# Performance work log

Hardware: AMD Instinct MI355X
Metric: run time of the kernel (lower is better)

Reference implementation:

```python
import jax, jax.numpy as jnp
import numpy as np

N_SRC = 100000
N_DST = 50000
N_EDGES = 1000000
D = 64
N_CLASSES = 64


def setup_inputs() -> dict:
    key = jax.random.key(0)
    ks = jax.random.split(key, 6)
    x = jax.random.normal(ks[0], (N_SRC, D), dtype=jnp.float32)
    w = jax.random.uniform(ks[1], (N_EDGES,), dtype=jnp.float32)
    u_sum = jax.random.uniform(ks[2], (N_SRC,), dtype=jnp.float32)
    W_w = jax.random.normal(ks[3], (N_CLASSES, 2 * D), dtype=jnp.float32) * (1.0 / np.sqrt(2 * D))
    W_b = jax.random.normal(ks[4], (N_CLASSES,), dtype=jnp.float32) * 0.01
    src_idx = jax.random.randint(ks[5], (N_EDGES,), 0, N_SRC, dtype=jnp.int64 if jax.config.jax_enable_x64 else jnp.int32)
    dst_idx = jax.random.randint(jax.random.fold_in(key, 7), (N_EDGES,), 0, N_DST, dtype=jnp.int64 if jax.config.jax_enable_x64 else jnp.int32)
    return {"x": x, "w": w, "u_sum": u_sum, "W_w": W_w, "W_b": W_b,
            "src_idx": src_idx, "dst_idx": dst_idx, "n_dst": N_DST}


def reference(x, w, u_sum, W_w, W_b, src_idx, dst_idx, n_dst):
    n_src, d = x.shape
    out_dim = W_w.shape[0]
    x_dst = x[:n_dst]                                  # dstdata['x']
    msgs = x[src_idx]                                  # [E, d] gather (u)
    # First update_all: u_mul_e + sum. NOTE: in the original module this result
    # is immediately overwritten by the second update_all, so it is dead math;
    # computed here for structural fidelity (XLA will DCE it).
    y_wsum = jax.ops.segment_sum(msgs * w[:, None], dst_idx, num_segments=n_dst)
    # Second update_all: copy_u + mean -> this is the 'y' actually used.
    deg = jax.ops.segment_sum(jnp.ones_like(w), dst_idx, num_segments=n_dst)
    y_mean = jax.ops.segment_sum(msgs, dst_idx, num_segments=n_dst) / jnp.maximum(deg, 1.0)[:, None]
    h = jnp.concatenate([x_dst, y_mean], axis=1) @ W_w.T + W_b  # [n_dst, out_dim]
    mean_x = jnp.mean(y_mean, axis=0)                  # [d]
    mean_u = u_sum / n_dst                             # [n_src]
    diff = mean_u[:, None] * x - mean_x                # [n_src, d]
    reg_loss = jnp.sum(diff * diff) / (n_src * out_dim)
    return h, reg_loss
```

## Files before the change

kernel.cpp:

```cpp
#include <hip/hip_runtime.h>

#define N_SRC   100000
#define N_DSTC  50000
#define N_EDGES 1000000
#define DIM     64
#define NCLS    64

#define SCAN_BPB 256
#define SCAN_NB  ((N_DSTC + SCAN_BPB - 1) / SCAN_BPB)

#define HIST_BLOCKS ((N_EDGES / 4 + 255) / 256)
#define REG_BLOCKS  1024
#define GATHER_GRID 1024


__global__ __launch_bounds__(256) void hist_reg_kernel(
    const int4*  __restrict__ dst4,
    const float* __restrict__ x,
    const float* __restrict__ u_sum,
    int*   __restrict__ hist,
    float* __restrict__ regA,
    float* __restrict__ regB) {
  __shared__ float redB[4][64];
  __shared__ float redA[4];

  if (blockIdx.x < HIST_BLOCKS) {
    int i = blockIdx.x * blockDim.x + threadIdx.x;
    if (i < N_EDGES / 4) {
      int4 d = dst4[i];
      atomicAdd(&hist[d.x], 1);
      atomicAdd(&hist[d.y], 1);
      atomicAdd(&hist[d.z], 1);
      atomicAdd(&hist[d.w], 1);
    }
    return;
  }

  const int tid  = threadIdx.x;
  const int wv   = tid >> 6;
  const int lane = tid & 63;
  const int waveId     = (blockIdx.x - HIST_BLOCKS) * 4 + wv;
  const int totalWaves = REG_BLOCKS * 4;

  float accA = 0.0f;
  float accB = 0.0f;
  for (int r = waveId; r < N_SRC; r += totalWaves) {
    float u  = u_sum[r];
    float xv = x[r * DIM + lane];
    float t  = u * xv;
    accB += t;
    accA = fmaf(t, t, accA);
  }
  #pragma unroll
  for (int off = 32; off > 0; off >>= 1)
    accA += __shfl_down(accA, off, 64);
  if (lane == 0) redA[wv] = accA;
  redB[wv][lane] = accB;
  __syncthreads();
  if (tid < 64) {
    float b = redB[0][tid] + redB[1][tid] + redB[2][tid] + redB[3][tid];
    atomicAdd(&regB[tid], b);
  }
  if (tid == 0) {
    float a = redA[0] + redA[1] + redA[2] + redA[3];
    atomicAdd(regA, a);
  }
}

__global__ __launch_bounds__(256) void scan_local(
    const int* __restrict__ hist, int* __restrict__ cursor,
    int* __restrict__ blockSums) {
  __shared__ int A[256], B[256];
  const int b = blockIdx.x, t = threadIdx.x;
  const int g = b * SCAN_BPB + t;
  int v = (g < N_DSTC) ? hist[g] : 0;
  A[t] = v;
  __syncthreads();
  int* cur = A; int* nxt = B;
  for (int off = 1; off < 256; off <<= 1) {
    int s = cur[t] + ((t >= off) ? cur[t - off] : 0);
    nxt[t] = s;
    __syncthreads();
    int* tmp = cur; cur = nxt; nxt = tmp;
  }
  if (g < N_DSTC) cursor[g] = cur[t] - v;
  if (t == 255) blockSums[b] = cur[255];
}

__global__ __launch_bounds__(256) void scan_addoff(
    int* __restrict__ cursor, const int* __restrict__ blockSums) {
  __shared__ int A[256], B[256];
  const int b = blockIdx.x, t = threadIdx.x;
  A[t] = (t < SCAN_NB) ? blockSums[t] : 0;
  __syncthreads();
  int* cur = A; int* nxt = B;
  for (int off = 1; off < 256; off <<= 1) {
    int s = cur[t] + ((t >= off) ? cur[t - off] : 0);
    nxt[t] = s;
    __syncthreads();
    int* tmp = cur; cur = nxt; nxt = tmp;
  }
  int off = (b > 0) ? cur[b - 1] : 0;
  int g = b * SCAN_BPB + t;
  if (g < N_DSTC) cursor[g] += off;
}

__global__ __launch_bounds__(256) void reorder_kernel(
    const int4* __restrict__ src4, const int4* __restrict__ dst4,
    int* __restrict__ cursor, int* __restrict__ sorted_src) {
  int i = blockIdx.x * blockDim.x + threadIdx.x;
  if (i < N_EDGES / 4) {
    int4 s = src4[i];
    int4 d = dst4[i];
    int p0 = atomicAdd(&cursor[d.x], 1); sorted_src[p0] = s.x;
    int p1 = atomicAdd(&cursor[d.y], 1); sorted_src[p1] = s.y;
    int p2 = atomicAdd(&cursor[d.z], 1); sorted_src[p2] = s.z;
    int p3 = atomicAdd(&cursor[d.w], 1); sorted_src[p3] = s.w;
  }
}

__global__ __launch_bounds__(256, 4) void gather_h(
    const float* __restrict__ x,
    const float* __restrict__ Ww,
    const float* __restrict__ Wb,
    const int*   __restrict__ cursor,
    const int*   __restrict__ sorted_src,
    float* __restrict__ h,
    float* __restrict__ colsum,
    float* __restrict__ regA,
    float* __restrict__ regB,
    int*   __restrict__ doneG,
    float* __restrict__ out_scalar) {
  __shared__ float Wt[2 * DIM][NCLS + 1];
  __shared__ float colred[4][64];
  __shared__ int   lastFlag;

  const int tid = threadIdx.x;
  for (int idx = tid; idx < NCLS * 2 * DIM; idx += 256) {
    int c = idx >> 7, k = idx & 127;
    Wt[k][c] = Ww[idx];
  }
  __syncthreads();

  const int wv   = tid >> 6;
  const int lane = tid & 63;
  const int es   = lane >> 4;
  const int q    = lane & 15;
  const int waveId = blockIdx.x * 4 + wv;
  const int tw     = gridDim.x * 4;
  const float bias = Wb[lane];
  const float4* x4 = reinterpret_cast<const float4*>(x);

  float4 colacc = make_float4(0.f, 0.f, 0.f, 0.f);

  for (int r = waveId; r < N_DSTC; r += tw) {
    int beg = (r == 0) ? 0 : cursor[r - 1];
    int end = cursor[r];
    int cnt = end - beg;

    float4 a = make_float4(0.f, 0.f, 0.f, 0.f);
    for (int base = 0; base < cnt; base += 64) {
      int rem = cnt - base;
      int mm  = rem < 64 ? rem : 64;
      int idxv = (lane < rem) ? sorted_src[beg + base + lane] : 0;

      int jb = 0;
      for (; jb + 8 <= mm; jb += 8) {
        int s0 = __shfl(idxv, jb + es,     64);
        int s1 = __shfl(idxv, jb + 4 + es, 64);
        float4 v0 = x4[s0 * 16 + q];
        float4 v1 = x4[s1 * 16 + q];
        a.x += v0.x + v1.x;
        a.y += v0.y + v1.y;
        a.z += v0.z + v1.z;
        a.w += v0.w + v1.w;
      }
      for (; jb < mm; jb += 4) {
        int j = jb + es;
        int s0 = __shfl(idxv, j & 63, 64);
        if (j < mm) {
          float4 v = x4[s0 * 16 + q];
          a.x += v.x; a.y += v.y; a.z += v.z; a.w += v.w;
        }
      }
    }
    a.x += __shfl_xor(a.x, 16, 64); a.y += __shfl_xor(a.y, 16, 64);
    a.z += __shfl_xor(a.z, 16, 64); a.w += __shfl_xor(a.w, 16, 64);
    a.x += __shfl_xor(a.x, 32, 64); a.y += __shfl_xor(a.y, 32, 64);
    a.z += __shfl_xor(a.z, 32, 64); a.w += __shfl_xor(a.w, 32, 64);

    float inv = 1.0f / fmaxf((float)cnt, 1.0f);
    float4 ym = make_float4(a.x * inv, a.y * inv, a.z * inv, a.w * inv);

    float4 xv = x4[r * 16 + q];

    if (es == 0) {
      colacc.x += ym.x; colacc.y += ym.y; colacc.z += ym.z; colacc.w += ym.w;
    }

    float hacc = bias;
    #pragma unroll
    for (int k = 0; k < DIM; ++k) {
      const int sl = k >> 2;
      float fx = __shfl((k & 3) == 0 ? xv.x : (k & 3) == 1 ? xv.y :
                        (k & 3) == 2 ? xv.z : xv.w, sl, 64);
      float fy = __shfl((k & 3) == 0 ? ym.x : (k & 3) == 1 ? ym.y :
                        (k & 3) == 2 ? ym.z : ym.w, sl, 64);
      hacc = fmaf(fx, Wt[k][lane], hacc);
      hacc = fmaf(fy, Wt[DIM + k][lane], hacc);
    }
    h[r * NCLS + lane] = hacc;
  }

  if (es == 0) {
    colred[wv][q * 4 + 0] = colacc.x;
    colred[wv][q * 4 + 1] = colacc.y;
    colred[wv][q * 4 + 2] = colacc.z;
    colred[wv][q * 4 + 3] = colacc.w;
  }
  __syncthreads();
  if (tid < 64) {
    float s = colred[0][tid] + colred[1][tid] + colred[2][tid] + colred[3][tid];
    atomicAdd(&colsum[tid], s);
  }

  __syncthreads();
  if (tid == 0) {
    __threadfence();
    int old = atomicAdd(doneG, 1);
    lastFlag = (old == (int)gridDim.x - 1) ? 1 : 0;
  }
  __syncthreads();
  if (lastFlag && tid < 64) {
    const float inv_nd = 1.0f / (float)N_DSTC;
    float cs = atomicAdd(&colsum[tid], 0.0f);
    float bv = atomicAdd(&regB[tid], 0.0f);
    float mx = cs * inv_nd;
    float p = fmaf((float)N_SRC * mx, mx, -2.0f * inv_nd * mx * bv);
    #pragma unroll
    for (int off = 32; off > 0; off >>= 1)
      p += __shfl_down(p, off, 64);
    if (tid == 0) {
      float av = atomicAdd(regA, 0.0f);
      float total = fmaf(av, inv_nd * inv_nd, p);
      out_scalar[0] = total * (1.0f / ((float)N_SRC * (float)NCLS));
    }
  }
}

extern "C" void kernel_launch(void* const* d_in, const int* in_sizes, int n_in,
                              void* d_out, int out_size, void* d_ws, size_t ws_size,
                              hipStream_t stream) {
  const float* x     = (const float*)d_in[0];
  const float* u_sum = (const float*)d_in[2];
  const float* Ww    = (const float*)d_in[3];
  const float* Wb    = (const float*)d_in[4];
  const int*   src   = (const int*)d_in[5];
  const int*   dst   = (const int*)d_in[6];

  float* out = (float*)d_out;
  int*   wsI = (int*)d_ws;

  int*   hist       = wsI;
  float* colsum     = (float*)(wsI + N_DSTC);
  float* regA       = colsum + 64;
  float* regB       = regA + 1;
  int*   doneG      = (int*)(regB + 64);
  int*   blockSums  = doneG + 1;
  int*   cursor     = blockSums + SCAN_NB;
  int*   sorted_src = cursor + N_DSTC;

  hipMemsetAsync(d_ws, 0, (size_t)(N_DSTC + 64 + 1 + 64 + 1) * sizeof(int), stream);

  hist_reg_kernel<<<HIST_BLOCKS + REG_BLOCKS, 256, 0, stream>>>(
      (const int4*)dst, x, u_sum, hist, regA, regB);
  scan_local  <<<SCAN_NB, 256, 0, stream>>>(hist, cursor, blockSums);
  scan_addoff <<<SCAN_NB, 256, 0, stream>>>(cursor, blockSums);
  reorder_kernel<<<(N_EDGES / 4 + 255) / 256, 256, 0, stream>>>(
      (const int4*)src, (const int4*)dst, cursor, sorted_src);
  gather_h    <<<GATHER_GRID, 256, 0, stream>>>(
      x, Ww, Wb, cursor, sorted_src, out, colsum, regA, regB, doneG,
      out + (size_t)N_DSTC * NCLS);
}
```

Before: 392.6 us.

## Gather neighbor features from a bf16 copy of x built in the reg pass

The reg-loss pass now also writes a round-to-nearest bf16 copy of x into workspace. The gather kernel reads that copy with 8 lanes per row and 8 rows per wave-step, which halves the bytes fetched per edge. It then reduces across lanes and redistributes one feature per lane before the linear layer. The gather grid is also doubled. The copy adds a write of about 12.8 MB, and summing bf16 values adds rounding error to the mean.

```diff
diff --git a/kernel.cpp b/kernel.cpp
--- a/kernel.cpp
+++ b/kernel.cpp
@@ -11,7 +11,7 @@
 
 #define HIST_BLOCKS ((N_EDGES / 4 + 255) / 256)
 #define REG_BLOCKS  1024
-#define GATHER_GRID 1024
+#define GATHER_GRID 2048
 
 
 __global__ __launch_bounds__(256) void hist_reg_kernel(
@@ -20,7 +20,8 @@
     const float* __restrict__ u_sum,
     int*   __restrict__ hist,
     float* __restrict__ regA,
-    float* __restrict__ regB) {
+    float* __restrict__ regB,
+    unsigned short* __restrict__ xh) {
   __shared__ float redB[4][64];
   __shared__ float redA[4];
 
@@ -47,6 +48,9 @@
   for (int r = waveId; r < N_SRC; r += totalWaves) {
     float u  = u_sum[r];
     float xv = x[r * DIM + lane];
+    unsigned int b = __float_as_uint(xv);
+    unsigned int rn = (b + 0x7fffu + ((b >> 16) & 1u)) >> 16;
+    xh[r * DIM + lane] = (unsigned short)rn;
     float t  = u * xv;
     accB += t;
     accA = fmaf(t, t, accA);
@@ -119,8 +123,16 @@
   }
 }
 
+__device__ __forceinline__ float bflo(unsigned int w) {
+  return __uint_as_float(w << 16);
+}
+__device__ __forceinline__ float bfhi(unsigned int w) {
+  return __uint_as_float(w & 0xffff0000u);
+}
+
 __global__ __launch_bounds__(256, 4) void gather_h(
     const float* __restrict__ x,
+    const unsigned short* __restrict__ xh,
     const float* __restrict__ Ww,
     const float* __restrict__ Wb,
     const int*   __restrict__ cursor,
@@ -144,80 +156,86 @@
 
   const int wv   = tid >> 6;
   const int lane = tid & 63;
-  const int es   = lane >> 4;
-  const int q    = lane & 15;
+  const int es   = lane >> 3;
+  const int q    = lane & 7;
   const int waveId = blockIdx.x * 4 + wv;
   const int tw     = gridDim.x * 4;
   const float bias = Wb[lane];
-  const float4* x4 = reinterpret_cast<const float4*>(x);
-
-  float4 colacc = make_float4(0.f, 0.f, 0.f, 0.f);
+  const uint4* xh4 = reinterpret_cast<const uint4*>(xh);
+
+  float colacc = 0.0f;
 
   for (int r = waveId; r < N_DSTC; r += tw) {
     int beg = (r == 0) ? 0 : cursor[r - 1];
     int end = cursor[r];
     int cnt = end - beg;
 
-    float4 a = make_float4(0.f, 0.f, 0.f, 0.f);
+    float a0 = 0.f, a1 = 0.f, a2 = 0.f, a3 = 0.f,
+          a4 = 0.f, a5 = 0.f, a6 = 0.f, a7 = 0.f;
     for (int base = 0; base < cnt; base += 64) {
       int rem = cnt - base;
       int mm  = rem < 64 ? rem : 64;
       int idxv = (lane < rem) ? sorted_src[beg + base + lane] : 0;
 
       int jb = 0;
-      for (; jb + 8 <= mm; jb += 8) {
+      for (; jb + 16 <= mm; jb += 16) {
         int s0 = __shfl(idxv, jb + es,     64);
-        int s1 = __shfl(idxv, jb + 4 + es, 64);
-        float4 v0 = x4[s0 * 16 + q];
-        float4 v1 = x4[s1 * 16 + q];
-        a.x += v0.x + v1.x;
-        a.y += v0.y + v1.y;
-        a.z += v0.z + v1.z;
-        a.w += v0.w + v1.w;
+        int s1 = __shfl(idxv, jb + 8 + es, 64);
+        uint4 w0 = xh4[s0 * 8 + q];
+        uint4 w1 = xh4[s1 * 8 + q];
+        a0 += bflo(w0.x) + bflo(w1.x);  a1 += bfhi(w0.x) + bfhi(w1.x);
+        a2 += bflo(w0.y) + bflo(w1.y);  a3 += bfhi(w0.y) + bfhi(w1.y);
+        a4 += bflo(w0.z) + bflo(w1.z);  a5 += bfhi(w0.z) + bfhi(w1.z);
+        a6 += bflo(w0.w) + bflo(w1.w);  a7 += bfhi(w0.w) + bfhi(w1.w);
       }
-      for (; jb < mm; jb += 4) {
+      for (; jb < mm; jb += 8) {
         int j = jb + es;
         int s0 = __shfl(idxv, j & 63, 64);
         if (j < mm) {
-          float4 v = x4[s0 * 16 + q];
-          a.x += v.x; a.y += v.y; a.z += v.z; a.w += v.w;
+          uint4 w0 = xh4[s0 * 8 + q];
+          a0 += bflo(w0.x);  a1 += bfhi(w0.x);
+          a2 += bflo(w0.y);  a3 += bfhi(w0.y);
+          a4 += bflo(w0.z);  a5 += bfhi(w0.z);
+          a6 += bflo(w0.w);  a7 += bfhi(w0.w);
         }
       }
     }
-    a.x += __shfl_xor(a.x, 16, 64); a.y += __shfl_xor(a.y, 16, 64);
-    a.z += __shfl_xor(a.z, 16, 64); a.w += __shfl_xor(a.w, 16, 64);
-    a.x += __shfl_xor(a.x, 32, 64); a.y += __shfl_xor(a.y, 32, 64);
-    a.z += __shfl_xor(a.z, 32, 64); a.w += __shfl_xor(a.w, 32, 64);
-
-    float inv = 1.0f / fmaxf((float)cnt, 1.0f);
-    float4 ym = make_float4(a.x * inv, a.y * inv, a.z * inv, a.w * inv);
-
-    float4 xv = x4[r * 16 + q];
-
-    if (es == 0) {
-      colacc.x += ym.x; colacc.y += ym.y; colacc.z += ym.z; colacc.w += ym.w;
-    }
+    #pragma unroll
+    for (int off = 8; off < 64; off <<= 1) {
+      a0 += __shfl_xor(a0, off, 64); a1 += __shfl_xor(a1, off, 64);
+      a2 += __shfl_xor(a2, off, 64); a3 += __shfl_xor(a3, off, 64);
+      a4 += __shfl_xor(a4, off, 64); a5 += __shfl_xor(a5, off, 64);
+      a6 += __shfl_xor(a6, off, 64); a7 += __shfl_xor(a7, off, 64);
+    }
+    const int srcl = lane >> 3;
+    float t0 = __shfl(a0, srcl, 64), t1 = __shfl(a1, srcl, 64);
+    float t2 = __shfl(a2, srcl, 64), t3 = __shfl(a3, srcl, 64);
+    float t4 = __shfl(a4, srcl, 64), t5 = __shfl(a5, srcl, 64);
+    float t6 = __shfl(a6, srcl, 64), t7 = __shfl(a7, srcl, 64);
+    const int sel = lane & 7;
+    float ysum = t0;
+    ysum = (sel == 1) ? t1 : ysum;  ysum = (sel == 2) ? t2 : ysum;
+    ysum = (sel == 3) ? t3 : ysum;  ysum = (sel == 4) ? t4 : ysum;
+    ysum = (sel == 5) ? t5 : ysum;  ysum = (sel == 6) ? t6 : ysum;
+    ysum = (sel == 7) ? t7 : ysum;
+
+    float ym = ysum / fmaxf((float)cnt, 1.0f);
+    colacc += ym;
+
+    float xv = x[r * DIM + lane];
 
     float hacc = bias;
     #pragma unroll
     for (int k = 0; k < DIM; ++k) {
-      const int sl = k >> 2;
-      float fx = __shfl((k & 3) == 0 ? xv.x : (k & 3) == 1 ? xv.y :
-                        (k & 3) == 2 ? xv.z : xv.w, sl, 64);
-      float fy = __shfl((k & 3) == 0 ? ym.x : (k & 3) == 1 ? ym.y :
-                        (k & 3) == 2 ? ym.z : ym.w, sl, 64);
+      float fx = __shfl(xv, k, 64);
+      float fy = __shfl(ym, k, 64);
       hacc = fmaf(fx, Wt[k][lane], hacc);
       hacc = fmaf(fy, Wt[DIM + k][lane], hacc);
     }
     h[r * NCLS + lane] = hacc;
   }
 
-  if (es == 0) {
-    colred[wv][q * 4 + 0] = colacc.x;
-    colred[wv][q * 4 + 1] = colacc.y;
-    colred[wv][q * 4 + 2] = colacc.z;
-    colred[wv][q * 4 + 3] = colacc.w;
-  }
+  colred[wv][lane] = colacc;
   __syncthreads();
   if (tid < 64) {
     float s = colred[0][tid] + colred[1][tid] + colred[2][tid] + colred[3][tid];
@@ -269,16 +287,17 @@
   int*   blockSums  = doneG + 1;
   int*   cursor     = blockSums + SCAN_NB;
   int*   sorted_src = cursor + N_DSTC;
+  unsigned short* xh = (unsigned short*)(wsI + 1100328);
 
   hipMemsetAsync(d_ws, 0, (size_t)(N_DSTC + 64 + 1 + 64 + 1) * sizeof(int), stream);
 
   hist_reg_kernel<<<HIST_BLOCKS + REG_BLOCKS, 256, 0, stream>>>(
-      (const int4*)dst, x, u_sum, hist, regA, regB);
+      (const int4*)dst, x, u_sum, hist, regA, regB, xh);
   scan_local  <<<SCAN_NB, 256, 0, stream>>>(hist, cursor, blockSums);
   scan_addoff <<<SCAN_NB, 256, 0, stream>>>(cursor, blockSums);
   reorder_kernel<<<(N_EDGES / 4 + 255) / 256, 256, 0, stream>>>(
       (const int4*)src, (const int4*)dst, cursor, sorted_src);
   gather_h    <<<GATHER_GRID, 256, 0, stream>>>(
-      x, Ww, Wb, cursor, sorted_src, out, colsum, regA, regB, doneG,
+      x, xh, Ww, Wb, cursor, sorted_src, out, colsum, regA, regB, doneG,
       out + (size_t)N_DSTC * NCLS);
 }
```

New measurement: 611.3 us. 55.7% more time.

## Gather neighbor features from a bf16 copy of x built in the histogram kernel

Applied to the files above, without the earlier changes.

The histogram blocks now also convert x to a packed bf16 copy in workspace. The gather kernel reads 8 bytes per lane instead of 16 for each neighbor row and accumulates in fp32, which halves the bytes moved by the random gather. The gather grid is also doubled to 2048 blocks. In exchange, the mean aggregation carries bf16 rounding error, and the conversion adds a full pass over x, reading 25.6MB and writing 12.8MB, in the first kernel.

```diff
diff --git a/kernel.cpp b/kernel.cpp
--- a/kernel.cpp
+++ b/kernel.cpp
@@ -11,8 +11,19 @@
 
 #define HIST_BLOCKS ((N_EDGES / 4 + 255) / 256)
 #define REG_BLOCKS  1024
-#define GATHER_GRID 1024
-
+#define GATHER_GRID 2048
+
+
+__device__ __forceinline__ unsigned int bf16rne(float f) {
+  unsigned int b = __float_as_uint(f);
+  return (b + 0x7fffu + ((b >> 16) & 1u)) >> 16;
+}
+__device__ __forceinline__ float bflo(unsigned int w) {
+  return __uint_as_float(w << 16);
+}
+__device__ __forceinline__ float bfhi(unsigned int w) {
+  return __uint_as_float(w & 0xffff0000u);
+}
 
 __global__ __launch_bounds__(256) void hist_reg_kernel(
     const int4*  __restrict__ dst4,
@@ -20,7 +31,8 @@
     const float* __restrict__ u_sum,
     int*   __restrict__ hist,
     float* __restrict__ regA,
-    float* __restrict__ regB) {
+    float* __restrict__ regB,
+    uint2* __restrict__ xh2) {
   __shared__ float redB[4][64];
   __shared__ float redA[4];
 
@@ -32,6 +44,15 @@
       atomicAdd(&hist[d.y], 1);
       atomicAdd(&hist[d.z], 1);
       atomicAdd(&hist[d.w], 1);
+    }
+    const float4* x4 = reinterpret_cast<const float4*>(x);
+    const int nv = N_SRC * DIM / 4;
+    for (int j = blockIdx.x * blockDim.x + threadIdx.x; j < nv;
+         j += HIST_BLOCKS * 256) {
+      float4 v = x4[j];
+      unsigned int lo = (bf16rne(v.y) << 16) | bf16rne(v.x);
+      unsigned int hi = (bf16rne(v.w) << 16) | bf16rne(v.z);
+      xh2[j] = make_uint2(lo, hi);
     }
     return;
   }
@@ -121,6 +142,7 @@
 
 __global__ __launch_bounds__(256, 4) void gather_h(
     const float* __restrict__ x,
+    const uint2* __restrict__ xh2,
     const float* __restrict__ Ww,
     const float* __restrict__ Wb,
     const int*   __restrict__ cursor,
@@ -165,22 +187,19 @@
       int idxv = (lane < rem) ? sorted_src[beg + base + lane] : 0;
 
       int jb = 0;
-      for (; jb + 8 <= mm; jb += 8) {
-        int s0 = __shfl(idxv, jb + es,     64);
-        int s1 = __shfl(idxv, jb + 4 + es, 64);
-        float4 v0 = x4[s0 * 16 + q];
-        float4 v1 = x4[s1 * 16 + q];
-        a.x += v0.x + v1.x;
-        a.y += v0.y + v1.y;
-        a.z += v0.z + v1.z;
-        a.w += v0.w + v1.w;
+      for (; jb + 4 <= mm; jb += 4) {
+        int s0 = __shfl(idxv, jb + es, 64);
+        uint2 w = xh2[s0 * 16 + q];
+        a.x += bflo(w.x);  a.y += bfhi(w.x);
+        a.z += bflo(w.y);  a.w += bfhi(w.y);
       }
       for (; jb < mm; jb += 4) {
         int j = jb + es;
         int s0 = __shfl(idxv, j & 63, 64);
         if (j < mm) {
-          float4 v = x4[s0 * 16 + q];
-          a.x += v.x; a.y += v.y; a.z += v.z; a.w += v.w;
+          uint2 w = xh2[s0 * 16 + q];
+          a.x += bflo(w.x);  a.y += bfhi(w.x);
+          a.z += bflo(w.y);  a.w += bfhi(w.y);
         }
       }
     }
@@ -269,16 +288,17 @@
   int*   blockSums  = doneG + 1;
   int*   cursor     = blockSums + SCAN_NB;
   int*   sorted_src = cursor + N_DSTC;
+  uint2* xh2        = (uint2*)(wsI + 1100328);
 
   hipMemsetAsync(d_ws, 0, (size_t)(N_DSTC + 64 + 1 + 64 + 1) * sizeof(int), stream);
 
   hist_reg_kernel<<<HIST_BLOCKS + REG_BLOCKS, 256, 0, stream>>>(
-      (const int4*)dst, x, u_sum, hist, regA, regB);
+      (const int4*)dst, x, u_sum, hist, regA, regB, xh2);
   scan_local  <<<SCAN_NB, 256, 0, stream>>>(hist, cursor, blockSums);
   scan_addoff <<<SCAN_NB, 256, 0, stream>>>(cursor, blockSums);
   reorder_kernel<<<(N_EDGES / 4 + 255) / 256, 256, 0, stream>>>(
       (const int4*)src, (const int4*)dst, cursor, sorted_src);
   gather_h    <<<GATHER_GRID, 256, 0, stream>>>(
-      x, Ww, Wb, cursor, sorted_src, out, colsum, regA, regB, doneG,
+      x, xh2, Ww, Wb, cursor, sorted_src, out, colsum, regA, regB, doneG,
       out + (size_t)N_DSTC * NCLS);
 }
```

New measurement: 422.2 us. +7.5%, slower.

## Bucket edges by source octile so all waves gather from the same x region together

Applied to the files above, without the earlier changes.

Sorts edges by a composite key (dst, src/6250) into 16 source buckets, and restructures the gather so each wave holds 13 destination-row accumulators in registers. It then walks bucket-by-bucket with a block barrier between buckets. The intent is to have the whole GPU gather from one slice of x at a time, so the working set stays cache-resident. In exchange, the histogram and scan grow 16x (800K keys, 1024-thread scan blocks), the accumulators raise register pressure, and the sync adds stalls. The workspace aliases sorted_src onto the hist buffer.

```diff
diff --git a/kernel.cpp b/kernel.cpp
--- a/kernel.cpp
+++ b/kernel.cpp
@@ -6,15 +6,22 @@
 #define DIM     64
 #define NCLS    64
 
-#define SCAN_BPB 256
-#define SCAN_NB  ((N_DSTC + SCAN_BPB - 1) / SCAN_BPB)
+#define NOCT    16
+#define OCT_DIV 6250
+#define NKEYS   (N_DSTC * NOCT)
+
+#define SCAN_BPB 1024
+#define SCAN_NB  ((NKEYS + SCAN_BPB - 1) / SCAN_BPB)
 
 #define HIST_BLOCKS ((N_EDGES / 4 + 255) / 256)
 #define REG_BLOCKS  1024
 #define GATHER_GRID 1024
+#define TOT_WAVES   (GATHER_GRID * 4)
+#define ROWS_PW     13
 
 
 __global__ __launch_bounds__(256) void hist_reg_kernel(
+    const int4*  __restrict__ src4,
     const int4*  __restrict__ dst4,
     const float* __restrict__ x,
     const float* __restrict__ u_sum,
@@ -27,11 +34,12 @@
   if (blockIdx.x < HIST_BLOCKS) {
     int i = blockIdx.x * blockDim.x + threadIdx.x;
     if (i < N_EDGES / 4) {
+      int4 s = src4[i];
       int4 d = dst4[i];
-      atomicAdd(&hist[d.x], 1);
-      atomicAdd(&hist[d.y], 1);
-      atomicAdd(&hist[d.z], 1);
-      atomicAdd(&hist[d.w], 1);
+      atomicAdd(&hist[d.x * NOCT + s.x / OCT_DIV], 1);
+      atomicAdd(&hist[d.y * NOCT + s.y / OCT_DIV], 1);
+      atomicAdd(&hist[d.z * NOCT + s.z / OCT_DIV], 1);
+      atomicAdd(&hist[d.w * NOCT + s.w / OCT_DIV], 1);
     }
     return;
   }
@@ -67,34 +75,34 @@
   }
 }
 
-__global__ __launch_bounds__(256) void scan_local(
+__global__ __launch_bounds__(1024) void scan_local(
     const int* __restrict__ hist, int* __restrict__ cursor,
     int* __restrict__ blockSums) {
-  __shared__ int A[256], B[256];
+  __shared__ int A[1024], B[1024];
   const int b = blockIdx.x, t = threadIdx.x;
   const int g = b * SCAN_BPB + t;
-  int v = (g < N_DSTC) ? hist[g] : 0;
+  int v = (g < NKEYS) ? hist[g] : 0;
   A[t] = v;
   __syncthreads();
   int* cur = A; int* nxt = B;
-  for (int off = 1; off < 256; off <<= 1) {
+  for (int off = 1; off < 1024; off <<= 1) {
     int s = cur[t] + ((t >= off) ? cur[t - off] : 0);
     nxt[t] = s;
     __syncthreads();
     int* tmp = cur; cur = nxt; nxt = tmp;
   }
-  if (g < N_DSTC) cursor[g] = cur[t] - v;
-  if (t == 255) blockSums[b] = cur[255];
-}
-
-__global__ __launch_bounds__(256) void scan_addoff(
+  if (g < NKEYS) cursor[g] = cur[t] - v;
+  if (t == 1023) blockSums[b] = cur[1023];
+}
+
+__global__ __launch_bounds__(1024) void scan_addoff(
     int* __restrict__ cursor, const int* __restrict__ blockSums) {
-  __shared__ int A[256], B[256];
+  __shared__ int A[1024], B[1024];
   const int b = blockIdx.x, t = threadIdx.x;
   A[t] = (t < SCAN_NB) ? blockSums[t] : 0;
   __syncthreads();
   int* cur = A; int* nxt = B;
-  for (int off = 1; off < 256; off <<= 1) {
+  for (int off = 1; off < 1024; off <<= 1) {
     int s = cur[t] + ((t >= off) ? cur[t - off] : 0);
     nxt[t] = s;
     __syncthreads();
@@ -102,7 +110,7 @@
   }
   int off = (b > 0) ? cur[b - 1] : 0;
   int g = b * SCAN_BPB + t;
-  if (g < N_DSTC) cursor[g] += off;
+  if (g < NKEYS) cursor[g] += off;
 }
 
 __global__ __launch_bounds__(256) void reorder_kernel(
@@ -112,10 +120,14 @@
   if (i < N_EDGES / 4) {
     int4 s = src4[i];
     int4 d = dst4[i];
-    int p0 = atomicAdd(&cursor[d.x], 1); sorted_src[p0] = s.x;
-    int p1 = atomicAdd(&cursor[d.y], 1); sorted_src[p1] = s.y;
-    int p2 = atomicAdd(&cursor[d.z], 1); sorted_src[p2] = s.z;
-    int p3 = atomicAdd(&cursor[d.w], 1); sorted_src[p3] = s.w;
+    int k0 = d.x * NOCT + s.x / OCT_DIV;
+    int k1 = d.y * NOCT + s.y / OCT_DIV;
+    int k2 = d.z * NOCT + s.z / OCT_DIV;
+    int k3 = d.w * NOCT + s.w / OCT_DIV;
+    int p0 = atomicAdd(&cursor[k0], 1); sorted_src[p0] = s.x;
+    int p1 = atomicAdd(&cursor[k1], 1); sorted_src[p1] = s.y;
+    int p2 = atomicAdd(&cursor[k2], 1); sorted_src[p2] = s.z;
+    int p3 = atomicAdd(&cursor[k3], 1); sorted_src[p3] = s.w;
   }
 }
 
@@ -147,69 +159,77 @@
   const int es   = lane >> 4;
   const int q    = lane & 15;
   const int waveId = blockIdx.x * 4 + wv;
-  const int tw     = gridDim.x * 4;
   const float bias = Wb[lane];
   const float4* x4 = reinterpret_cast<const float4*>(x);
 
-  float4 colacc = make_float4(0.f, 0.f, 0.f, 0.f);
-
-  for (int r = waveId; r < N_DSTC; r += tw) {
-    int beg = (r == 0) ? 0 : cursor[r - 1];
-    int end = cursor[r];
-    int cnt = end - beg;
-
-    float4 a = make_float4(0.f, 0.f, 0.f, 0.f);
-    for (int base = 0; base < cnt; base += 64) {
-      int rem = cnt - base;
-      int mm  = rem < 64 ? rem : 64;
-      int idxv = (lane < rem) ? sorted_src[beg + base + lane] : 0;
-
-      int jb = 0;
-      for (; jb + 8 <= mm; jb += 8) {
-        int s0 = __shfl(idxv, jb + es,     64);
-        int s1 = __shfl(idxv, jb + 4 + es, 64);
-        float4 v0 = x4[s0 * 16 + q];
-        float4 v1 = x4[s1 * 16 + q];
-        a.x += v0.x + v1.x;
-        a.y += v0.y + v1.y;
-        a.z += v0.z + v1.z;
-        a.w += v0.w + v1.w;
-      }
-      for (; jb < mm; jb += 4) {
-        int j = jb + es;
-        int s0 = __shfl(idxv, j & 63, 64);
-        if (j < mm) {
-          float4 v = x4[s0 * 16 + q];
-          a.x += v.x; a.y += v.y; a.z += v.z; a.w += v.w;
+  float4 acc[ROWS_PW];
+  #pragma unroll
+  for (int j = 0; j < ROWS_PW; ++j) acc[j] = make_float4(0.f, 0.f, 0.f, 0.f);
+
+  for (int oc = 0; oc < NOCT; ++oc) {
+    #pragma unroll
+    for (int j = 0; j < ROWS_PW; ++j) {
+      int r = waveId + j * TOT_WAVES;
+      if (r < N_DSTC) {
+        int key = r * NOCT + oc;
+        int beg = (key == 0) ? 0 : cursor[key - 1];
+        int end = cursor[key];
+        int cnt = end - beg;
+        for (int base = 0; base < cnt; base += 64) {
+          int rem = cnt - base;
+          int mm  = rem < 64 ? rem : 64;
+          int idxv = (lane < rem) ? sorted_src[beg + base + lane] : 0;
+          for (int jb = 0; jb < mm; jb += 4) {
+            int jj = jb + es;
+            int s0 = __shfl(idxv, jj & 63, 64);
+            if (jj < mm) {
+              float4 v = x4[s0 * 16 + q];
+              acc[j].x += v.x; acc[j].y += v.y;
+              acc[j].z += v.z; acc[j].w += v.w;
+            }
+          }
         }
       }
     }
-    a.x += __shfl_xor(a.x, 16, 64); a.y += __shfl_xor(a.y, 16, 64);
-    a.z += __shfl_xor(a.z, 16, 64); a.w += __shfl_xor(a.w, 16, 64);
-    a.x += __shfl_xor(a.x, 32, 64); a.y += __shfl_xor(a.y, 32, 64);
-    a.z += __shfl_xor(a.z, 32, 64); a.w += __shfl_xor(a.w, 32, 64);
-
-    float inv = 1.0f / fmaxf((float)cnt, 1.0f);
-    float4 ym = make_float4(a.x * inv, a.y * inv, a.z * inv, a.w * inv);
-
-    float4 xv = x4[r * 16 + q];
-
-    if (es == 0) {
-      colacc.x += ym.x; colacc.y += ym.y; colacc.z += ym.z; colacc.w += ym.w;
+    __syncthreads();
+  }
+
+  float4 colacc = make_float4(0.f, 0.f, 0.f, 0.f);
+  #pragma unroll
+  for (int j = 0; j < ROWS_PW; ++j) {
+    int r = waveId + j * TOT_WAVES;
+    if (r < N_DSTC) {
+      float4 a = acc[j];
+      a.x += __shfl_xor(a.x, 16, 64); a.y += __shfl_xor(a.y, 16, 64);
+      a.z += __shfl_xor(a.z, 16, 64); a.w += __shfl_xor(a.w, 16, 64);
+      a.x += __shfl_xor(a.x, 32, 64); a.y += __shfl_xor(a.y, 32, 64);
+      a.z += __shfl_xor(a.z, 32, 64); a.w += __shfl_xor(a.w, 32, 64);
+
+      int begR = (r == 0) ? 0 : cursor[r * NOCT - 1];
+      int cnt  = cursor[r * NOCT + (NOCT - 1)] - begR;
+      float inv = 1.0f / fmaxf((float)cnt, 1.0f);
+      float4 ym = make_float4(a.x * inv, a.y * inv, a.z * inv, a.w * inv);
+
+      float4 xv = x4[r * 16 + q];
+
+      if (es == 0) {
+        colacc.x += ym.x; colacc.y += ym.y;
+        colacc.z += ym.z; colacc.w += ym.w;
+      }
+
+      float hacc = bias;
+      #pragma unroll
+      for (int k = 0; k < DIM; ++k) {
+        const int sl = k >> 2;
+        float fx = __shfl((k & 3) == 0 ? xv.x : (k & 3) == 1 ? xv.y :
+                          (k & 3) == 2 ? xv.z : xv.w, sl, 64);
+        float fy = __shfl((k & 3) == 0 ? ym.x : (k & 3) == 1 ? ym.y :
+                          (k & 3) == 2 ? ym.z : ym.w, sl, 64);
+        hacc = fmaf(fx, Wt[k][lane], hacc);
+        hacc = fmaf(fy, Wt[DIM + k][lane], hacc);
+      }
+      h[r * NCLS + lane] = hacc;
     }
-
-    float hacc = bias;
-    #pragma unroll
-    for (int k = 0; k < DIM; ++k) {
-      const int sl = k >> 2;
-      float fx = __shfl((k & 3) == 0 ? xv.x : (k & 3) == 1 ? xv.y :
-                        (k & 3) == 2 ? xv.z : xv.w, sl, 64);
-      float fy = __shfl((k & 3) == 0 ? ym.x : (k & 3) == 1 ? ym.y :
-                        (k & 3) == 2 ? ym.z : ym.w, sl, 64);
-      hacc = fmaf(fx, Wt[k][lane], hacc);
-      hacc = fmaf(fy, Wt[DIM + k][lane], hacc);
-    }
-    h[r * NCLS + lane] = hacc;
   }
 
   if (es == 0) {
@@ -261,21 +281,22 @@
   float* out = (float*)d_out;
   int*   wsI = (int*)d_ws;
 
+  int*   sorted_src = wsI;
   int*   hist       = wsI;
-  float* colsum     = (float*)(wsI + N_DSTC);
+  float* colsum     = (float*)(wsI + 1000000);
   float* regA       = colsum + 64;
   float* regB       = regA + 1;
   int*   doneG      = (int*)(regB + 64);
   int*   blockSums  = doneG + 1;
   int*   cursor     = blockSums + SCAN_NB;
-  int*   sorted_src = cursor + N_DSTC;
-
-  hipMemsetAsync(d_ws, 0, (size_t)(N_DSTC + 64 + 1 + 64 + 1) * sizeof(int), stream);
+
+  hipMemsetAsync(hist, 0, (size_t)NKEYS * sizeof(int), stream);
+  hipMemsetAsync(colsum, 0, (size_t)(64 + 1 + 64 + 1) * sizeof(int), stream);
 
   hist_reg_kernel<<<HIST_BLOCKS + REG_BLOCKS, 256, 0, stream>>>(
-      (const int4*)dst, x, u_sum, hist, regA, regB);
-  scan_local  <<<SCAN_NB, 256, 0, stream>>>(hist, cursor, blockSums);
-  scan_addoff <<<SCAN_NB, 256, 0, stream>>>(cursor, blockSums);
+      (const int4*)src, (const int4*)dst, x, u_sum, hist, regA, regB);
+  scan_local  <<<SCAN_NB, 1024, 0, stream>>>(hist, cursor, blockSums);
+  scan_addoff <<<SCAN_NB, 1024, 0, stream>>>(cursor, blockSums);
   reorder_kernel<<<(N_EDGES / 4 + 255) / 256, 256, 0, stream>>>(
       (const int4*)src, (const int4*)dst, cursor, sorted_src);
   gather_h    <<<GATHER_GRID, 256, 0, stream>>>(
```

New measurement: 516.0 us. 31.4% more time.
